# Performance work log

Measured on AMD Instinct MI355X. Metric: run time of the kernel, lower is better.

The kernel has to match this reference:

```python
import jax, jax.numpy as jnp
import numpy as np

B, C_IN, H, W = 8, 32, 64, 64
C = 64  # num_channels


def setup_inputs() -> dict:
    key = jax.random.key(0)
    ks = jax.random.split(key, 9)
    s_in = 1.0 / np.sqrt(C_IN)
    s_c = 1.0 / np.sqrt(C)
    return {
        "x": jax.random.normal(ks[0], (B, C_IN, H, W), dtype=jnp.float32),
        "wq": jax.random.uniform(ks[1], (C, C_IN), jnp.float32, -s_in, s_in),
        "bq": jax.random.uniform(ks[2], (C,), jnp.float32, -s_in, s_in),
        "wk": jax.random.uniform(ks[3], (C, C_IN), jnp.float32, -s_in, s_in),
        "bk": jax.random.uniform(ks[4], (C,), jnp.float32, -s_in, s_in),
        "wv": jax.random.uniform(ks[5], (C, C_IN), jnp.float32, -s_in, s_in),
        "bv": jax.random.uniform(ks[6], (C,), jnp.float32, -s_in, s_in),
        "wo": jax.random.uniform(ks[7], (C_IN, C), jnp.float32, -s_c, s_c),
        "bo": jax.random.uniform(ks[8], (C_IN,), jnp.float32, -s_c, s_c),
    }


def reference(x, wq, bq, wk, bk, wv, bv, wo, bo):
    b, c_in, h, w = x.shape
    n = h * w
    # 1x1 convs == per-pixel linear projections; produce (B, N, C) directly
    q = (jnp.einsum('bchw,oc->bhwo', x, wq) + bq).reshape(b, n, -1)
    k = (jnp.einsum('bchw,oc->bhwo', x, wk) + bk).reshape(b, n, -1)
    v = (jnp.einsum('bchw,oc->bhwo', x, wv) + bv).reshape(b, n, -1)
    # unscaled attention over spatial positions (no 1/sqrt(d) in original)
    scores = jnp.einsum('bnc,bmc->bnm', q, k)  # (B, N, N)
    attn = jax.nn.softmax(scores, axis=-1)
    out = jnp.einsum('bnm,bmc->bnc', attn, v)  # (B, N, C)
    out = out.reshape(b, h, w, -1)
    out = jnp.einsum('bhwc,oc->bohw', out, wo) + bo[None, :, None, None]
    return out + x
```

## Files before the change

kernel.cpp:

```cpp
#include <hip/hip_runtime.h>
#include <hip/hip_bf16.h>

#define CIN    32
#define NPIX   4096
#define DIM    64
#define LOG2E  1.4426950408889634f

#if __has_builtin(__builtin_amdgcn_exp2f)
#define EXP2(x) __builtin_amdgcn_exp2f(x)
#else
#define EXP2(x) exp2f(x)
#endif

typedef float  f32x4 __attribute__((ext_vector_type(4)));
typedef short  s16x8 __attribute__((ext_vector_type(8)));

__device__ __forceinline__ unsigned short bf16_bits(float f) {
    union { __hip_bfloat16 h; unsigned short u; } cv;
    cv.h = __float2bfloat16(f);
    return cv.u;
}


__global__ __launch_bounds__(256) void qkv_proj(
    const float* __restrict__ x,
    const float* __restrict__ wq, const float* __restrict__ bq,
    const float* __restrict__ wk, const float* __restrict__ bk,
    const float* __restrict__ wv, const float* __restrict__ bv,
    __hip_bfloat16* __restrict__ qb, __hip_bfloat16* __restrict__ kb,
    __hip_bfloat16* __restrict__ vb)
{
    __shared__ float Xs[CIN][64];
    __shared__ float wT[3][CIN][DIM];

    const int tid = threadIdx.x;
    const int b   = blockIdx.y;
    const int bx  = blockIdx.x;
    const int n0  = bx * 64;

    for (int i = tid; i < 3 * CIN * DIM; i += 256) {
        int m = i >> 11, r = i & 2047, c = r >> 6, o = r & 63;
        const float* wsrc = (m == 0) ? wq : (m == 1) ? wk : wv;
        float wv0 = wsrc[o * CIN + c];
        wT[m][c][o] = (m == 0) ? wv0 * LOG2E : wv0;
    }
    for (int i = tid * 4; i < CIN * 64; i += 1024) {
        int c = i >> 6, p = i & 63;
        *(f32x4*)&Xs[c][p] = *(const f32x4*)&x[((size_t)b * CIN + c) * NPIX + n0 + p];
    }
    __syncthreads();

    const int w    = tid >> 6;
    const int lane = tid & 63;
    const int l16  = lane >> 2;
    const int quad = lane & 3;

    const int T  = bx * 4 + w;
    const int px = T * 16 + l16;

    float aq[2][8], ak[2][8];
    #pragma unroll
    for (int kb2 = 0; kb2 < 2; kb2++) {
        f32x4 bq0 = *(const f32x4*)&bq[kb2 * 32 + quad * 8];
        f32x4 bq1 = *(const f32x4*)&bq[kb2 * 32 + quad * 8 + 4];
        f32x4 bk0 = *(const f32x4*)&bk[kb2 * 32 + quad * 8];
        f32x4 bk1 = *(const f32x4*)&bk[kb2 * 32 + quad * 8 + 4];
        #pragma unroll
        for (int j = 0; j < 4; j++) {
            aq[kb2][j] = bq0[j] * LOG2E; aq[kb2][j + 4] = bq1[j] * LOG2E;
            ak[kb2][j] = bk0[j];         ak[kb2][j + 4] = bk1[j];
        }
    }
    #pragma unroll 8
    for (int c = 0; c < CIN; c++) {
        const float xc = Xs[c][w * 16 + l16];
        #pragma unroll
        for (int kb2 = 0; kb2 < 2; kb2++) {
            f32x4 q0 = *(const f32x4*)&wT[0][c][kb2 * 32 + quad * 8];
            f32x4 q1 = *(const f32x4*)&wT[0][c][kb2 * 32 + quad * 8 + 4];
            f32x4 k0 = *(const f32x4*)&wT[1][c][kb2 * 32 + quad * 8];
            f32x4 k1 = *(const f32x4*)&wT[1][c][kb2 * 32 + quad * 8 + 4];
            #pragma unroll
            for (int j = 0; j < 4; j++) {
                aq[kb2][j]     += xc * q0[j];
                aq[kb2][j + 4] += xc * q1[j];
                ak[kb2][j]     += xc * k0[j];
                ak[kb2][j + 4] += xc * k1[j];
            }
        }
    }
    #pragma unroll
    for (int kb2 = 0; kb2 < 2; kb2++) {
        union { s16x8 v; __hip_bfloat16 h[8]; } pq, pk;
        #pragma unroll
        for (int j = 0; j < 8; j++) {
            pq.h[j] = __float2bfloat16(aq[kb2][j]);
            pk.h[j] = __float2bfloat16(ak[kb2][j]);
        }
        *(s16x8*)(qb + ((size_t)b * NPIX + px) * DIM + kb2 * 32 + quad * 8) = pq.v;
        const size_t koff =
            ((((size_t)(b * 256 + T) * 2 + kb2) * 16 + l16) * 4 + quad) * 8;
        *(s16x8*)(kb + koff) = pk.v;
    }

    const int ch = w * 16 + l16;
    float av[2][8];
    {
        const float bvc = bv[ch];
        #pragma unroll
        for (int kh = 0; kh < 2; kh++)
            #pragma unroll
            for (int j = 0; j < 8; j++) av[kh][j] = bvc;
    }
    #pragma unroll 8
    for (int c = 0; c < CIN; c++) {
        const float wvc = wT[2][c][ch];
        f32x4 x0 = *(const f32x4*)&Xs[c][quad * 8];
        f32x4 x1 = *(const f32x4*)&Xs[c][quad * 8 + 4];
        f32x4 x2 = *(const f32x4*)&Xs[c][32 + quad * 8];
        f32x4 x3 = *(const f32x4*)&Xs[c][32 + quad * 8 + 4];
        #pragma unroll
        for (int j = 0; j < 4; j++) {
            av[0][j]     += x0[j] * wvc;
            av[0][j + 4] += x1[j] * wvc;
            av[1][j]     += x2[j] * wvc;
            av[1][j + 4] += x3[j] * wvc;
        }
    }
    #pragma unroll
    for (int kh = 0; kh < 2; kh++) {
        union { s16x8 v; __hip_bfloat16 h[8]; } pv;
        #pragma unroll
        for (int j = 0; j < 8; j++) pv.h[j] = __float2bfloat16(av[kh][j]);
        const size_t voff =
            (((((size_t)(b * 64 + bx) * 2 + kh) * 4 + w) * 16 + l16) * 4 + quad) * 8;
        *(s16x8*)(vb + voff) = pv.v;
    }
}

#define PM_OFF   0
#define RED_OFF  0
#define LRED_OFF 50688
#define ON_OFF   51456
#define SMEM_SZ  60672

__global__ __launch_bounds__(256, 2) void attn_fused(
    const __hip_bfloat16* __restrict__ qb,
    const __hip_bfloat16* __restrict__ kbf,
    const __hip_bfloat16* __restrict__ vbf,
    const float* __restrict__ wo, const float* __restrict__ bo,
    const float* __restrict__ x, float* __restrict__ y)
{
    __shared__ __align__(16) char smem[SMEM_SZ];

    const int tid  = threadIdx.x;
    const int kq   = tid >> 6;
    const int lane = tid & 63;
    const int quad = lane >> 4, l16 = lane & 15;
    const int b    = blockIdx.x;
    const int row0 = blockIdx.y * 64;

    s16x8 qf[4][2];
    #pragma unroll
    for (int mt = 0; mt < 4; mt++)
        #pragma unroll
        for (int kb2 = 0; kb2 < 2; kb2++)
            qf[mt][kb2] = *(const s16x8*)(qb
                + ((size_t)b * NPIX + row0 + mt * 16 + l16) * DIM + kb2 * 32 + quad * 8);

    const f32x4 zero4 = {0.f, 0.f, 0.f, 0.f};
    f32x4 o[4][4];
    #pragma unroll
    for (int mt = 0; mt < 4; mt++)
        #pragma unroll
        for (int ct = 0; ct < 4; ct++) o[mt][ct] = zero4;
    f32x4 ol[4] = {zero4, zero4, zero4, zero4};

    s16x8 ones;
    #pragma unroll
    for (int j = 0; j < 8; j++) ones[j] = (short)0x3F80;

    const char* kp = (const char*)kbf + (size_t)b * 524288 + kq * 131072
                     + (l16 * 4 + quad) * 16;
    const char* vp = (const char*)vbf + (size_t)b * 524288 + kq * 131072
                     + (l16 * 4 + quad) * 16;
    char* pmw = smem + PM_OFF + kq * 4608;

    s16x8 ckA[4], cvA[4], ckB[4], cvB[4];
    #pragma unroll
    for (int i = 0; i < 4; i++) {
        ckA[i] = *(const s16x8*)(kp + i * 1024);
        cvA[i] = *(const s16x8*)(vp + i * 1024);
    }

    auto step = [&](s16x8 (&curK)[4], s16x8 (&curV)[4],
                    s16x8 (&nxtK)[4], s16x8 (&nxtV)[4]) {
        kp += 4096; vp += 4096;
        f32x4 st[2][4];
        #pragma unroll
        for (int nt = 0; nt < 2; nt++)
            #pragma unroll
            for (int mt = 0; mt < 4; mt++) {
                st[nt][mt] = __builtin_amdgcn_mfma_f32_16x16x32_bf16(
                    curK[nt * 2 + 0], qf[mt][0], zero4, 0, 0, 0);
                st[nt][mt] = __builtin_amdgcn_mfma_f32_16x16x32_bf16(
                    curK[nt * 2 + 1], qf[mt][1], st[nt][mt], 0, 0, 0);
            }
        #pragma unroll
        for (int i = 0; i < 4; i++) nxtK[i] = *(const s16x8*)(kp + i * 1024);

        #pragma unroll
        for (int nt = 0; nt < 2; nt++)
            #pragma unroll
            for (int mt = 0; mt < 4; mt++) {
                f32x4 p = st[nt][mt];
                #pragma unroll
                for (int r = 0; r < 4; r++) p[r] = EXP2(p[r]);
                unsigned int d0 = (__float_as_uint(p[1]) & 0xffff0000u)
                                | (__float_as_uint(p[0]) >> 16);
                unsigned int d1 = (__float_as_uint(p[3]) & 0xffff0000u)
                                | (__float_as_uint(p[2]) >> 16);
                unsigned long long dd = ((unsigned long long)d1 << 32) | d0;
                *(unsigned long long*)(pmw + (mt * 16 + l16) * 72 + nt * 32 + quad * 8) = dd;
            }
        s16x8 pf[4];
        #pragma unroll
        for (int mt = 0; mt < 4; mt++)
            pf[mt] = *(const s16x8*)(pmw + (mt * 16 + l16) * 72 + quad * 16);

        #pragma unroll
        for (int ct = 0; ct < 4; ct++)
            #pragma unroll
            for (int mt = 0; mt < 4; mt++)
                o[mt][ct] = __builtin_amdgcn_mfma_f32_16x16x32_bf16(
                    pf[mt], curV[ct], o[mt][ct], 0, 0, 0);
        #pragma unroll
        for (int mt = 0; mt < 4; mt++)
            ol[mt] = __builtin_amdgcn_mfma_f32_16x16x32_bf16(
                pf[mt], ones, ol[mt], 0, 0, 0);
        #pragma unroll
        for (int i = 0; i < 4; i++) nxtV[i] = *(const s16x8*)(vp + i * 1024);
    };

    for (int it = 0; it < 16; it++) {
        step(ckA, cvA, ckB, cvB);
        step(ckB, cvB, ckA, cvA);
    }

    __syncthreads();

    float* RED  = (float*)(smem + RED_OFF);
    float* LRED = (float*)(smem + LRED_OFF);

    if (kq != 0) {
        float* R = RED + (kq - 1) * 64 * 66;
        float* L = LRED + (kq - 1) * 64;
        #pragma unroll
        for (int mt = 0; mt < 4; mt++) {
            #pragma unroll
            for (int ct = 0; ct < 4; ct++)
                #pragma unroll
                for (int r = 0; r < 4; r++)
                    R[(mt * 16 + quad * 4 + r) * 66 + ct * 16 + l16] = o[mt][ct][r];
            if (l16 == 0)
                #pragma unroll
                for (int r = 0; r < 4; r++)
                    L[mt * 16 + quad * 4 + r] = ol[mt][r];
        }
    }
    __syncthreads();

    if (kq == 0) {
        #pragma unroll
        for (int reg = 0; reg < 3; reg++) {
            const float* R = RED + reg * 64 * 66;
            const float* L = LRED + reg * 64;
            #pragma unroll
            for (int mt = 0; mt < 4; mt++)
                #pragma unroll
                for (int r = 0; r < 4; r++) {
                    ol[mt][r] += L[mt * 16 + quad * 4 + r];
                    #pragma unroll
                    for (int ct = 0; ct < 4; ct++)
                        o[mt][ct][r] += R[(mt * 16 + quad * 4 + r) * 66 + ct * 16 + l16];
                }
        }

        __hip_bfloat16* ON = (__hip_bfloat16*)(smem + ON_OFF);
        #pragma unroll
        for (int mt = 0; mt < 4; mt++)
            #pragma unroll
            for (int r = 0; r < 4; r++) {
                const float inv = 1.0f / ol[mt][r];
                #pragma unroll
                for (int ct = 0; ct < 4; ct++)
                    ON[(mt * 16 + quad * 4 + r) * 72 + ct * 16 + l16]
                        = __float2bfloat16(o[mt][ct][r] * inv);
            }
        s16x8 af[4][2];
        #pragma unroll
        for (int mt = 0; mt < 4; mt++)
            #pragma unroll
            for (int kb2 = 0; kb2 < 2; kb2++)
                af[mt][kb2] = *(const s16x8*)(ON + (mt * 16 + l16) * 72
                                              + kb2 * 32 + quad * 8);

        f32x4 d[4][2];
        #pragma unroll
        for (int mt = 0; mt < 4; mt++)
            #pragma unroll
            for (int nt = 0; nt < 2; nt++) d[mt][nt] = zero4;
        #pragma unroll
        for (int nt = 0; nt < 2; nt++)
            #pragma unroll
            for (int kb2 = 0; kb2 < 2; kb2++) {
                const float* wp = wo + (size_t)(nt * 16 + l16) * DIM + kb2 * 32 + quad * 8;
                union { s16x8 v; __hip_bfloat16 h[8]; } wf;
                #pragma unroll
                for (int j = 0; j < 8; j++) wf.h[j] = __float2bfloat16(wp[j]);
                #pragma unroll
                for (int mt = 0; mt < 4; mt++)
                    d[mt][nt] = __builtin_amdgcn_mfma_f32_16x16x32_bf16(
                        af[mt][kb2], wf.v, d[mt][nt], 0, 0, 0);
            }

        #pragma unroll
        for (int nt = 0; nt < 2; nt++) {
            const int out = nt * 16 + l16;
            const float bias = bo[out];
            #pragma unroll
            for (int mt = 0; mt < 4; mt++)
                #pragma unroll
                for (int r = 0; r < 4; r++) {
                    const int row = row0 + mt * 16 + quad * 4 + r;
                    const size_t xi = ((size_t)b * CIN + out) * NPIX + row;
                    y[xi] = d[mt][nt][r] + bias + x[xi];
                }
        }
    }
}

extern "C" void kernel_launch(void* const* d_in, const int* in_sizes, int n_in,
                              void* d_out, int out_size, void* d_ws, size_t ws_size,
                              hipStream_t stream)
{
    const float* x  = (const float*)d_in[0];
    const float* wq = (const float*)d_in[1];
    const float* bq = (const float*)d_in[2];
    const float* wk = (const float*)d_in[3];
    const float* bk = (const float*)d_in[4];
    const float* wv = (const float*)d_in[5];
    const float* bv = (const float*)d_in[6];
    const float* wo = (const float*)d_in[7];
    const float* bo = (const float*)d_in[8];
    float* y = (float*)d_out;

    char* ws = (char*)d_ws;
    __hip_bfloat16* qb = (__hip_bfloat16*)(ws);
    __hip_bfloat16* kb = (__hip_bfloat16*)(ws + (4u << 20));
    __hip_bfloat16* vb = (__hip_bfloat16*)(ws + (8u << 20));

    qkv_proj<<<dim3(64, 8), dim3(256), 0, stream>>>(x, wq, bq, wk, bk, wv, bv, qb, kb, vb);
    attn_fused<<<dim3(8, 64), dim3(256), 0, stream>>>(qb, kb, vb, wo, bo, x, y);
}
```

Baseline: 135.1 us.

## Halve query tile per block, double grid, and software-pipeline QK/PV stages

Each attention block now handles 32 query rows instead of 64, doubling the grid to 1024 blocks and raising the occupancy hint to 3 blocks per CU. Shared memory shrinks, and the row-sum partials move into a spare column of the reduction buffer. The main loop is reordered so the QK MFMAs of one tile overlap the PV MFMAs of the previous tile, with single-buffered K/V register fragments. The cost is that every block streams the full K/V, so K/V global traffic doubles relative to the compute done per block.

```diff
diff --git a/kernel.cpp b/kernel.cpp
--- a/kernel.cpp
+++ b/kernel.cpp
@@ -140,11 +140,10 @@
 
 #define PM_OFF   0
 #define RED_OFF  0
-#define LRED_OFF 50688
-#define ON_OFF   51456
-#define SMEM_SZ  60672
-
-__global__ __launch_bounds__(256, 2) void attn_fused(
+#define ON_OFF   25344
+#define SMEM_SZ  29952
+
+__global__ __launch_bounds__(256, 3) void attn_fused(
     const __hip_bfloat16* __restrict__ qb,
     const __hip_bfloat16* __restrict__ kbf,
     const __hip_bfloat16* __restrict__ vbf,
@@ -158,23 +157,23 @@
     const int lane = tid & 63;
     const int quad = lane >> 4, l16 = lane & 15;
     const int b    = blockIdx.x;
-    const int row0 = blockIdx.y * 64;
-
-    s16x8 qf[4][2];
-    #pragma unroll
-    for (int mt = 0; mt < 4; mt++)
+    const int row0 = blockIdx.y * 32;
+
+    s16x8 qf[2][2];
+    #pragma unroll
+    for (int mt = 0; mt < 2; mt++)
         #pragma unroll
         for (int kb2 = 0; kb2 < 2; kb2++)
             qf[mt][kb2] = *(const s16x8*)(qb
                 + ((size_t)b * NPIX + row0 + mt * 16 + l16) * DIM + kb2 * 32 + quad * 8);
 
     const f32x4 zero4 = {0.f, 0.f, 0.f, 0.f};
-    f32x4 o[4][4];
-    #pragma unroll
-    for (int mt = 0; mt < 4; mt++)
+    f32x4 o[2][4];
+    #pragma unroll
+    for (int mt = 0; mt < 2; mt++)
         #pragma unroll
         for (int ct = 0; ct < 4; ct++) o[mt][ct] = zero4;
-    f32x4 ol[4] = {zero4, zero4, zero4, zero4};
+    f32x4 ol[2] = {zero4, zero4};
 
     s16x8 ones;
     #pragma unroll
@@ -184,35 +183,27 @@
                      + (l16 * 4 + quad) * 16;
     const char* vp = (const char*)vbf + (size_t)b * 524288 + kq * 131072
                      + (l16 * 4 + quad) * 16;
-    char* pmw = smem + PM_OFF + kq * 4608;
-
-    s16x8 ckA[4], cvA[4], ckB[4], cvB[4];
-    #pragma unroll
-    for (int i = 0; i < 4; i++) {
-        ckA[i] = *(const s16x8*)(kp + i * 1024);
-        cvA[i] = *(const s16x8*)(vp + i * 1024);
-    }
-
-    auto step = [&](s16x8 (&curK)[4], s16x8 (&curV)[4],
-                    s16x8 (&nxtK)[4], s16x8 (&nxtV)[4]) {
-        kp += 4096; vp += 4096;
-        f32x4 st[2][4];
+    char* pmw = smem + PM_OFF + kq * 2304;
+
+    s16x8 ckf[4], cvf[4], pf[2];
+    f32x4 st[2][2];
+
+    auto compute_st = [&]() {
         #pragma unroll
         for (int nt = 0; nt < 2; nt++)
             #pragma unroll
-            for (int mt = 0; mt < 4; mt++) {
+            for (int mt = 0; mt < 2; mt++) {
                 st[nt][mt] = __builtin_amdgcn_mfma_f32_16x16x32_bf16(
-                    curK[nt * 2 + 0], qf[mt][0], zero4, 0, 0, 0);
+                    ckf[nt * 2 + 0], qf[mt][0], zero4, 0, 0, 0);
                 st[nt][mt] = __builtin_amdgcn_mfma_f32_16x16x32_bf16(
-                    curK[nt * 2 + 1], qf[mt][1], st[nt][mt], 0, 0, 0);
-            }
-        #pragma unroll
-        for (int i = 0; i < 4; i++) nxtK[i] = *(const s16x8*)(kp + i * 1024);
-
+                    ckf[nt * 2 + 1], qf[mt][1], st[nt][mt], 0, 0, 0);
+            }
+    };
+    auto pack_write = [&]() {
         #pragma unroll
         for (int nt = 0; nt < 2; nt++)
             #pragma unroll
-            for (int mt = 0; mt < 4; mt++) {
+            for (int mt = 0; mt < 2; mt++) {
                 f32x4 p = st[nt][mt];
                 #pragma unroll
                 for (int r = 0; r < 4; r++) p[r] = EXP2(p[r]);
@@ -223,40 +214,60 @@
                 unsigned long long dd = ((unsigned long long)d1 << 32) | d0;
                 *(unsigned long long*)(pmw + (mt * 16 + l16) * 72 + nt * 32 + quad * 8) = dd;
             }
-        s16x8 pf[4];
-        #pragma unroll
-        for (int mt = 0; mt < 4; mt++)
+    };
+    auto read_pf = [&]() {
+        #pragma unroll
+        for (int mt = 0; mt < 2; mt++)
             pf[mt] = *(const s16x8*)(pmw + (mt * 16 + l16) * 72 + quad * 16);
-
+    };
+    auto do_pv = [&]() {
         #pragma unroll
         for (int ct = 0; ct < 4; ct++)
             #pragma unroll
-            for (int mt = 0; mt < 4; mt++)
+            for (int mt = 0; mt < 2; mt++)
                 o[mt][ct] = __builtin_amdgcn_mfma_f32_16x16x32_bf16(
-                    pf[mt], curV[ct], o[mt][ct], 0, 0, 0);
-        #pragma unroll
-        for (int mt = 0; mt < 4; mt++)
+                    pf[mt], cvf[ct], o[mt][ct], 0, 0, 0);
+        #pragma unroll
+        for (int mt = 0; mt < 2; mt++)
             ol[mt] = __builtin_amdgcn_mfma_f32_16x16x32_bf16(
                 pf[mt], ones, ol[mt], 0, 0, 0);
-        #pragma unroll
-        for (int i = 0; i < 4; i++) nxtV[i] = *(const s16x8*)(vp + i * 1024);
-    };
-
-    for (int it = 0; it < 16; it++) {
-        step(ckA, cvA, ckB, cvB);
-        step(ckB, cvB, ckA, cvA);
-    }
+    };
+    auto load_k = [&](int it) {
+        #pragma unroll
+        for (int i = 0; i < 4; i++)
+            ckf[i] = *(const s16x8*)(kp + (size_t)it * 4096 + i * 1024);
+    };
+    auto load_v = [&](int it) {
+        #pragma unroll
+        for (int i = 0; i < 4; i++)
+            cvf[i] = *(const s16x8*)(vp + (size_t)it * 4096 + i * 1024);
+    };
+
+    load_k(0);
+    compute_st();
+    load_k(1);
+    pack_write();
+    read_pf();
+    load_v(0);
+
+    for (int it = 1; it < 32; it++) {
+        compute_st();
+        load_k(it + 1);
+        do_pv();
+        pack_write();
+        read_pf();
+        load_v(it);
+    }
+    do_pv();
 
     __syncthreads();
 
-    float* RED  = (float*)(smem + RED_OFF);
-    float* LRED = (float*)(smem + LRED_OFF);
+    float* RED = (float*)(smem + RED_OFF);
 
     if (kq != 0) {
-        float* R = RED + (kq - 1) * 64 * 66;
-        float* L = LRED + (kq - 1) * 64;
-        #pragma unroll
-        for (int mt = 0; mt < 4; mt++) {
+        float* R = RED + (kq - 1) * 32 * 66;
+        #pragma unroll
+        for (int mt = 0; mt < 2; mt++) {
             #pragma unroll
             for (int ct = 0; ct < 4; ct++)
                 #pragma unroll
@@ -265,7 +276,7 @@
             if (l16 == 0)
                 #pragma unroll
                 for (int r = 0; r < 4; r++)
-                    L[mt * 16 + quad * 4 + r] = ol[mt][r];
+                    R[(mt * 16 + quad * 4 + r) * 66 + 64] = ol[mt][r];
         }
     }
     __syncthreads();
@@ -273,13 +284,12 @@
     if (kq == 0) {
         #pragma unroll
         for (int reg = 0; reg < 3; reg++) {
-            const float* R = RED + reg * 64 * 66;
-            const float* L = LRED + reg * 64;
-            #pragma unroll
-            for (int mt = 0; mt < 4; mt++)
+            const float* R = RED + reg * 32 * 66;
+            #pragma unroll
+            for (int mt = 0; mt < 2; mt++)
                 #pragma unroll
                 for (int r = 0; r < 4; r++) {
-                    ol[mt][r] += L[mt * 16 + quad * 4 + r];
+                    ol[mt][r] += R[(mt * 16 + quad * 4 + r) * 66 + 64];
                     #pragma unroll
                     for (int ct = 0; ct < 4; ct++)
                         o[mt][ct][r] += R[(mt * 16 + quad * 4 + r) * 66 + ct * 16 + l16];
@@ -288,7 +298,7 @@
 
         __hip_bfloat16* ON = (__hip_bfloat16*)(smem + ON_OFF);
         #pragma unroll
-        for (int mt = 0; mt < 4; mt++)
+        for (int mt = 0; mt < 2; mt++)
             #pragma unroll
             for (int r = 0; r < 4; r++) {
                 const float inv = 1.0f / ol[mt][r];
@@ -297,19 +307,15 @@
                     ON[(mt * 16 + quad * 4 + r) * 72 + ct * 16 + l16]
                         = __float2bfloat16(o[mt][ct][r] * inv);
             }
-        s16x8 af[4][2];
-        #pragma unroll
-        for (int mt = 0; mt < 4; mt++)
+        s16x8 af[2][2];
+        #pragma unroll
+        for (int mt = 0; mt < 2; mt++)
             #pragma unroll
             for (int kb2 = 0; kb2 < 2; kb2++)
                 af[mt][kb2] = *(const s16x8*)(ON + (mt * 16 + l16) * 72
                                               + kb2 * 32 + quad * 8);
 
-        f32x4 d[4][2];
-        #pragma unroll
-        for (int mt = 0; mt < 4; mt++)
-            #pragma unroll
-            for (int nt = 0; nt < 2; nt++) d[mt][nt] = zero4;
+        f32x4 d[2][2] = {{zero4, zero4}, {zero4, zero4}};
         #pragma unroll
         for (int nt = 0; nt < 2; nt++)
             #pragma unroll
@@ -319,7 +325,7 @@
                 #pragma unroll
                 for (int j = 0; j < 8; j++) wf.h[j] = __float2bfloat16(wp[j]);
                 #pragma unroll
-                for (int mt = 0; mt < 4; mt++)
+                for (int mt = 0; mt < 2; mt++)
                     d[mt][nt] = __builtin_amdgcn_mfma_f32_16x16x32_bf16(
                         af[mt][kb2], wf.v, d[mt][nt], 0, 0, 0);
             }
@@ -329,7 +335,7 @@
             const int out = nt * 16 + l16;
             const float bias = bo[out];
             #pragma unroll
-            for (int mt = 0; mt < 4; mt++)
+            for (int mt = 0; mt < 2; mt++)
                 #pragma unroll
                 for (int r = 0; r < 4; r++) {
                     const int row = row0 + mt * 16 + quad * 4 + r;
@@ -361,5 +367,5 @@
     __hip_bfloat16* vb = (__hip_bfloat16*)(ws + (8u << 20));
 
     qkv_proj<<<dim3(64, 8), dim3(256), 0, stream>>>(x, wq, bq, wk, bk, wv, bv, qb, kb, vb);
-    attn_fused<<<dim3(8, 64), dim3(256), 0, stream>>>(qb, kb, vb, wo, bo, x, y);
+    attn_fused<<<dim3(8, 128), dim3(256), 0, stream>>>(qb, kb, vb, wo, bo, x, y);
 }
```

Measured after the change: 153.0 us. 13.3% more time.

## Split key range across eight waves with tree reduction of partial outputs

Applied to the files above, without the earlier changes.

The attention block now launches 512 threads (8 waves), each handling 512 keys instead of 1024, so a block's key loop is half as long and more waves are available to hide MFMA and memory latency. Partial O and row-sum accumulators are combined through a three-level shared-memory tree reduction in place of a serial reduction into wave 0. This adds extra barriers and a larger LDS footprint, and the launch bounds of 512 threads with 4 blocks per CU may force register spilling given the large per-thread accumulator and fragment state.

```diff
diff --git a/kernel.cpp b/kernel.cpp
--- a/kernel.cpp
+++ b/kernel.cpp
@@ -138,13 +138,11 @@
     }
 }
 
-#define PM_OFF   0
-#define RED_OFF  0
-#define LRED_OFF 50688
-#define ON_OFF   51456
-#define SMEM_SZ  60672
-
-__global__ __launch_bounds__(256, 2) void attn_fused(
+#define RSTRIDE 66
+#define RBUF    (64 * RSTRIDE)
+#define SMEM_SZ 67584
+
+__global__ __launch_bounds__(512, 4) void attn_fused(
     const __hip_bfloat16* __restrict__ qb,
     const __hip_bfloat16* __restrict__ kbf,
     const __hip_bfloat16* __restrict__ vbf,
@@ -154,7 +152,7 @@
     __shared__ __align__(16) char smem[SMEM_SZ];
 
     const int tid  = threadIdx.x;
-    const int kq   = tid >> 6;
+    const int w    = tid >> 6;
     const int lane = tid & 63;
     const int quad = lane >> 4, l16 = lane & 15;
     const int b    = blockIdx.x;
@@ -180,11 +178,11 @@
     #pragma unroll
     for (int j = 0; j < 8; j++) ones[j] = (short)0x3F80;
 
-    const char* kp = (const char*)kbf + (size_t)b * 524288 + kq * 131072
+    const char* kp = (const char*)kbf + (size_t)b * 524288 + w * 65536
                      + (l16 * 4 + quad) * 16;
-    const char* vp = (const char*)vbf + (size_t)b * 524288 + kq * 131072
+    const char* vp = (const char*)vbf + (size_t)b * 524288 + w * 65536
                      + (l16 * 4 + quad) * 16;
-    char* pmw = smem + PM_OFF + kq * 4608;
+    char* pmw = smem + w * 4608;
 
     s16x8 ckA[4], cvA[4], ckB[4], cvB[4];
     #pragma unroll
@@ -242,51 +240,57 @@
         for (int i = 0; i < 4; i++) nxtV[i] = *(const s16x8*)(vp + i * 1024);
     };
 
-    for (int it = 0; it < 16; it++) {
+    for (int it = 0; it < 8; it++) {
         step(ckA, cvA, ckB, cvB);
         step(ckB, cvB, ckA, cvA);
     }
 
-    __syncthreads();
-
-    float* RED  = (float*)(smem + RED_OFF);
-    float* LRED = (float*)(smem + LRED_OFF);
-
-    if (kq != 0) {
-        float* R = RED + (kq - 1) * 64 * 66;
-        float* L = LRED + (kq - 1) * 64;
+    float* RED = (float*)smem;
+
+    auto dump = [&](int bufid) {
+        float* R = RED + bufid * RBUF;
         #pragma unroll
         for (int mt = 0; mt < 4; mt++) {
             #pragma unroll
             for (int ct = 0; ct < 4; ct++)
                 #pragma unroll
                 for (int r = 0; r < 4; r++)
-                    R[(mt * 16 + quad * 4 + r) * 66 + ct * 16 + l16] = o[mt][ct][r];
+                    R[(mt * 16 + quad * 4 + r) * RSTRIDE + ct * 16 + l16] = o[mt][ct][r];
             if (l16 == 0)
                 #pragma unroll
                 for (int r = 0; r < 4; r++)
-                    L[mt * 16 + quad * 4 + r] = ol[mt][r];
-        }
-    }
-    __syncthreads();
-
-    if (kq == 0) {
-        #pragma unroll
-        for (int reg = 0; reg < 3; reg++) {
-            const float* R = RED + reg * 64 * 66;
-            const float* L = LRED + reg * 64;
-            #pragma unroll
-            for (int mt = 0; mt < 4; mt++)
-                #pragma unroll
-                for (int r = 0; r < 4; r++) {
-                    ol[mt][r] += L[mt * 16 + quad * 4 + r];
-                    #pragma unroll
-                    for (int ct = 0; ct < 4; ct++)
-                        o[mt][ct][r] += R[(mt * 16 + quad * 4 + r) * 66 + ct * 16 + l16];
-                }
-        }
-
-        __hip_bfloat16* ON = (__hip_bfloat16*)(smem + ON_OFF);
+                    R[(mt * 16 + quad * 4 + r) * RSTRIDE + 64] = ol[mt][r];
+        }
+    };
+    auto accum = [&](int bufid) {
+        const float* R = RED + bufid * RBUF;
+        #pragma unroll
+        for (int mt = 0; mt < 4; mt++)
+            #pragma unroll
+            for (int r = 0; r < 4; r++) {
+                ol[mt][r] += R[(mt * 16 + quad * 4 + r) * RSTRIDE + 64];
+                #pragma unroll
+                for (int ct = 0; ct < 4; ct++)
+                    o[mt][ct][r] += R[(mt * 16 + quad * 4 + r) * RSTRIDE + ct * 16 + l16];
+            }
+    };
+
+    __syncthreads();
+    if (w >= 4) dump(w - 4);
+    __syncthreads();
+    if (w < 4) accum(w);
+    __syncthreads();
+    if (w == 2 || w == 3) dump(w - 2);
+    __syncthreads();
+    if (w < 2) accum(w);
+    __syncthreads();
+    if (w == 1) dump(0);
+    __syncthreads();
+
+    if (w == 0) {
+        accum(0);
+
+        __hip_bfloat16* ON = (__hip_bfloat16*)smem;
         #pragma unroll
         for (int mt = 0; mt < 4; mt++)
             #pragma unroll
@@ -361,5 +365,5 @@
     __hip_bfloat16* vb = (__hip_bfloat16*)(ws + (8u << 20));
 
     qkv_proj<<<dim3(64, 8), dim3(256), 0, stream>>>(x, wq, bq, wk, bk, wv, bv, qb, kb, vb);
-    attn_fused<<<dim3(8, 64), dim3(256), 0, stream>>>(qb, kb, vb, wo, bo, x, y);
+    attn_fused<<<dim3(8, 64), dim3(512), 0, stream>>>(qb, kb, vb, wo, bo, x, y);
 }
```

Result: slower. 325.3 us (+140.9%).

## Software-pipeline attention loop so PV MFMAs overlap next tile's QK and exp

Applied to the files above, without the earlier changes.

Restructures the flash-attention inner loop into a skewed pipeline. The P·V MFMAs of the previous tile now run between the QK^T MFMAs and the exp/pack of the current tile, which lets matrix work overlap the transcendental and LDS traffic. V is now single-buffered and loaded one step later, which frees registers. The row-sum reduction buffer is folded into a spare column of the padded RED rows, removing the separate LRED region. This costs an explicit prologue and epilogue, and the reordering could add register pressure or LDS hazards under the 2-blocks-per-CU launch bound.

```diff
diff --git a/kernel.cpp b/kernel.cpp
--- a/kernel.cpp
+++ b/kernel.cpp
@@ -140,7 +140,6 @@
 
 #define PM_OFF   0
 #define RED_OFF  0
-#define LRED_OFF 50688
 #define ON_OFF   51456
 #define SMEM_SZ  60672
 
@@ -186,17 +185,10 @@
                      + (l16 * 4 + quad) * 16;
     char* pmw = smem + PM_OFF + kq * 4608;
 
-    s16x8 ckA[4], cvA[4], ckB[4], cvB[4];
-    #pragma unroll
-    for (int i = 0; i < 4; i++) {
-        ckA[i] = *(const s16x8*)(kp + i * 1024);
-        cvA[i] = *(const s16x8*)(vp + i * 1024);
-    }
-
-    auto step = [&](s16x8 (&curK)[4], s16x8 (&curV)[4],
-                    s16x8 (&nxtK)[4], s16x8 (&nxtV)[4]) {
-        kp += 4096; vp += 4096;
-        f32x4 st[2][4];
+    s16x8 ckA[4], ckB[4], cvf[4], pf[4];
+    f32x4 st[2][4];
+
+    auto compute_st = [&](s16x8 (&curK)[4]) {
         #pragma unroll
         for (int nt = 0; nt < 2; nt++)
             #pragma unroll
@@ -206,9 +198,18 @@
                 st[nt][mt] = __builtin_amdgcn_mfma_f32_16x16x32_bf16(
                     curK[nt * 2 + 1], qf[mt][1], st[nt][mt], 0, 0, 0);
             }
-        #pragma unroll
-        for (int i = 0; i < 4; i++) nxtK[i] = *(const s16x8*)(kp + i * 1024);
-
+    };
+    auto load_k = [&](s16x8 (&dst)[4], int it) {
+        #pragma unroll
+        for (int i = 0; i < 4; i++)
+            dst[i] = *(const s16x8*)(kp + (size_t)it * 4096 + i * 1024);
+    };
+    auto load_v = [&](int it) {
+        #pragma unroll
+        for (int i = 0; i < 4; i++)
+            cvf[i] = *(const s16x8*)(vp + (size_t)it * 4096 + i * 1024);
+    };
+    auto pack_write = [&]() {
         #pragma unroll
         for (int nt = 0; nt < 2; nt++)
             #pragma unroll
@@ -223,38 +224,54 @@
                 unsigned long long dd = ((unsigned long long)d1 << 32) | d0;
                 *(unsigned long long*)(pmw + (mt * 16 + l16) * 72 + nt * 32 + quad * 8) = dd;
             }
-        s16x8 pf[4];
+    };
+    auto read_pf = [&]() {
         #pragma unroll
         for (int mt = 0; mt < 4; mt++)
             pf[mt] = *(const s16x8*)(pmw + (mt * 16 + l16) * 72 + quad * 16);
-
+    };
+    auto do_pv = [&]() {
         #pragma unroll
         for (int ct = 0; ct < 4; ct++)
             #pragma unroll
             for (int mt = 0; mt < 4; mt++)
                 o[mt][ct] = __builtin_amdgcn_mfma_f32_16x16x32_bf16(
-                    pf[mt], curV[ct], o[mt][ct], 0, 0, 0);
+                    pf[mt], cvf[ct], o[mt][ct], 0, 0, 0);
         #pragma unroll
         for (int mt = 0; mt < 4; mt++)
             ol[mt] = __builtin_amdgcn_mfma_f32_16x16x32_bf16(
                 pf[mt], ones, ol[mt], 0, 0, 0);
-        #pragma unroll
-        for (int i = 0; i < 4; i++) nxtV[i] = *(const s16x8*)(vp + i * 1024);
-    };
-
-    for (int it = 0; it < 16; it++) {
-        step(ckA, cvA, ckB, cvB);
-        step(ckB, cvB, ckA, cvA);
-    }
+    };
+
+    auto step = [&](s16x8 (&curK)[4], s16x8 (&nxtK)[4], int it) {
+        compute_st(curK);
+        load_k(nxtK, it + 1);
+        do_pv();
+        pack_write();
+        read_pf();
+        load_v(it);
+    };
+
+    load_k(ckA, 0);
+    load_v(0);
+    compute_st(ckA);
+    load_k(ckB, 1);
+    pack_write();
+    read_pf();
+
+    for (int it = 1; it < 31; it += 2) {
+        step(ckB, ckA, it);
+        step(ckA, ckB, it + 1);
+    }
+    step(ckB, ckA, 31);
+    do_pv();
 
     __syncthreads();
 
-    float* RED  = (float*)(smem + RED_OFF);
-    float* LRED = (float*)(smem + LRED_OFF);
+    float* RED = (float*)(smem + RED_OFF);
 
     if (kq != 0) {
         float* R = RED + (kq - 1) * 64 * 66;
-        float* L = LRED + (kq - 1) * 64;
         #pragma unroll
         for (int mt = 0; mt < 4; mt++) {
             #pragma unroll
@@ -265,7 +282,7 @@
             if (l16 == 0)
                 #pragma unroll
                 for (int r = 0; r < 4; r++)
-                    L[mt * 16 + quad * 4 + r] = ol[mt][r];
+                    R[(mt * 16 + quad * 4 + r) * 66 + 64] = ol[mt][r];
         }
     }
     __syncthreads();
@@ -274,12 +291,11 @@
         #pragma unroll
         for (int reg = 0; reg < 3; reg++) {
             const float* R = RED + reg * 64 * 66;
-            const float* L = LRED + reg * 64;
             #pragma unroll
             for (int mt = 0; mt < 4; mt++)
                 #pragma unroll
                 for (int r = 0; r < 4; r++) {
-                    ol[mt][r] += L[mt * 16 + quad * 4 + r];
+                    ol[mt][r] += R[(mt * 16 + quad * 4 + r) * 66 + 64];
                     #pragma unroll
                     for (int ct = 0; ct < 4; ct++)
                         o[mt][ct][r] += R[(mt * 16 + quad * 4 + r) * 66 + ct * 16 + l16];
```

After: 135.3 us. About the same (+0.2%).
